# Kernel optimization log

Hardware: AMD Instinct MI355X
Metric: run time of the kernel (lower is better)

The kernel has to match this reference:

```python
import jax, jax.numpy as jnp
import numpy as np

NUM_EXPERTS = 64
N_GROUP = 8
TOPK_GROUP = 4
TOPK = 8
EPG = NUM_EXPERTS // N_GROUP  # experts per group


def setup_inputs() -> dict:
    key = jax.random.key(0)
    k1, k2 = jax.random.split(key)
    S, D = 16384, 2048
    x = jax.random.normal(k1, (S, D), dtype=jnp.float32)
    # nn.Linear(n_embd, num_experts, bias=False) weight: [E, D]
    W = jax.random.normal(k2, (NUM_EXPERTS, D), dtype=jnp.float32) * (1.0 / np.sqrt(D))
    e_score_correction_bias = jnp.zeros((NUM_EXPERTS,), dtype=jnp.float32)
    return {"x": x, "W": W, "e_score_correction_bias": e_score_correction_bias}


def reference(x, W, e_score_correction_bias):
    S = x.shape[0]
    E, G, K = NUM_EXPERTS, N_GROUP, TOPK
    # router projection in fp32
    logits = jnp.einsum('sd,ed->se', x.astype(jnp.float32), W)  # [S, E]
    scores = jax.nn.sigmoid(logits).astype(x.dtype)             # [S, E]
    scores_biased = scores + e_score_correction_bias            # [S, E]
    # group max over experts-per-group
    group_scores = scores_biased.reshape(S, G, EPG).max(axis=-1)  # [S, G]
    _, selected_group = jax.lax.top_k(group_scores, TOPK_GROUP)   # [S, topk_group]
    # build group mask via scatter (faithful to scatter_ of ones)
    group_mask = jnp.zeros((S, G), dtype=scores_biased.dtype)
    group_mask = group_mask.at[jnp.arange(S)[:, None], selected_group].set(1.0)
    expert_mask = jnp.broadcast_to(group_mask[:, :, None], (S, G, EPG)).reshape(S, E)
    scores_masked = jnp.where(expert_mask == 0, -jnp.inf, scores_biased)
    _, topk_idx = jax.lax.top_k(scores_masked, K)               # [S, K]
    final_weights = jnp.take_along_axis(scores, topk_idx, axis=1)  # [S, K]
    # norm_topk_prob=True
    final_weights = final_weights / (final_weights.sum(axis=-1, keepdims=True) + 1e-20)
    return (topk_idx, final_weights)
```

## Files before the change

### kernel.cpp

```cpp
#include <hip/hip_runtime.h>
#include <math.h>

#define N_EXP 64
#define TOPK 8
#define TOPK_G 4
#define D_DIM 2048
#define S_TOT 16384
#define RPB 64
#define NBUF 4
#define NCH 32

typedef _Float16 half8 __attribute__((ext_vector_type(8)));
typedef float f32x4 __attribute__((ext_vector_type(4)));

typedef __attribute__((address_space(1))) const unsigned int ga_u32;
typedef __attribute__((address_space(3))) unsigned int ls_u32;
#define GLL(src, dst) \
    __builtin_amdgcn_global_load_lds((ga_u32*)(src), (ls_u32*)(dst), 16, 0, 0)
#define VM(n) asm volatile("s_waitcnt vmcnt(" #n ")" ::: "memory")
#define BAR() do { asm volatile("" ::: "memory"); \
                   __builtin_amdgcn_s_barrier(); \
                   asm volatile("" ::: "memory"); } while (0)

__global__ void split_w_kernel(const float* __restrict__ W,
                               _Float16* __restrict__ wsg) {
    int t = blockIdx.x * blockDim.x + threadIdx.x;
    if (t >= 16384) return;
    const int c   = t >> 9;
    const int kh  = (t >> 8) & 1;
    const int t4  = (t >> 6) & 3;
    const int m16 = (t >> 2) & 15;
    const int kb  = t & 3;
    const int slot = (kb + (m16 >> 1)) & 3;
    _Float16* dh = wsg + (size_t)c * 8192 + (kh * 4 + t4) * 512 + m16 * 32 + slot * 8;
    _Float16* dl = dh + 4096;
    const float* s = W + (size_t)(t4 * 16 + m16) * D_DIM + c * 64 + kh * 32 + kb * 8;
#pragma unroll
    for (int i = 0; i < 8; ++i) {
        float f = s[i];
        _Float16 h = (_Float16)f;
        dh[i] = h;
        dl[i] = (_Float16)((f - (float)h) * 2048.0f);
    }
}

__launch_bounds__(1024)
__global__ void router_kernel(const float* __restrict__ x,
                              const _Float16* __restrict__ wsg,
                              const float* __restrict__ bias,
                              float* __restrict__ out_idx,
                              float* __restrict__ out_w)
{
    __shared__ __align__(16) float    xs[NBUF][4096];
    __shared__ __align__(16) _Float16 wh[NBUF][8192];

    const int tid  = threadIdx.x;
    const int w    = tid >> 6;
    const int et   = w & 3;
    const int kh   = (w >> 2) & 1;
    const int rh   = w >> 3;
    const int lane = tid & 63;
    const int m16  = lane & 15;
    const int kb   = lane >> 4;
    const int row0 = blockIdx.x * RPB;

    const int gidx = tid;
    const int gr = gidx >> 4;
    const int gs = gidx & 15;
    const int gh = gs >> 3;
    const int gq = ((gs & 7) - gr) & 7;
    const float*    xsrc = x + (size_t)(row0 + gr) * D_DIM + gh * 32 + gq * 4;
    const _Float16* wsrc = wsg + (size_t)tid * 8;

#define STAGE(c, b) do { \
        GLL(xsrc + (size_t)(c) * 64, &xs[b][w * 256]); \
        GLL(wsrc + (size_t)(c) * 8192, &wh[b][w * 512]); \
    } while (0)

    f32x4 accHH[2], accHL[2], accLH[2];
#pragma unroll
    for (int mt = 0; mt < 2; ++mt) {
        accHH[mt] = (f32x4)0.0f; accHL[mt] = (f32x4)0.0f; accLH[mt] = (f32x4)0.0f;
    }

#define COMPUTE(b) do { \
        const int boff = (kh * 4 + et) * 512 + m16 * 32 + ((kb + (m16 >> 1)) & 3) * 8; \
        const half8 bh = *(const half8*)&wh[b][boff]; \
        const half8 bl = *(const half8*)&wh[b][4096 + boff]; \
        _Pragma("unroll") \
        for (int mt = 0; mt < 2; ++mt) { \
            const int rr = rh * 32 + mt * 16 + m16; \
            const int p0 = rr * 16 + kh * 8 + ((kb * 2 + rr) & 7); \
            const int p1 = rr * 16 + kh * 8 + ((kb * 2 + 1 + rr) & 7); \
            const float4 f0 = *(const float4*)&xs[b][p0 * 4]; \
            const float4 f1 = *(const float4*)&xs[b][p1 * 4]; \
            const float v[8] = {f0.x, f0.y, f0.z, f0.w, f1.x, f1.y, f1.z, f1.w}; \
            half8 xh, xl; \
            _Pragma("unroll") \
            for (int i = 0; i < 8; ++i) { \
                _Float16 h = (_Float16)v[i]; \
                xh[i] = h; \
                xl[i] = (_Float16)((v[i] - (float)h) * 2048.0f); \
            } \
            accHH[mt] = __builtin_amdgcn_mfma_f32_16x16x32_f16(xh, bh, accHH[mt], 0, 0, 0); \
            accHL[mt] = __builtin_amdgcn_mfma_f32_16x16x32_f16(xh, bl, accHL[mt], 0, 0, 0); \
            accLH[mt] = __builtin_amdgcn_mfma_f32_16x16x32_f16(xl, bh, accLH[mt], 0, 0, 0); \
        } \
    } while (0)

    STAGE(0, 0); STAGE(1, 1);

    for (int c = 0; c < NCH; ++c) {
        if (c + 2 < NCH)        { STAGE(c + 2, (c + 2) & 3); VM(4); }
        else if (c == NCH - 2)  VM(2);
        else                    VM(0);
        BAR();
        COMPUTE(c & 3);
    }
#undef STAGE
#undef COMPUTE
    BAR();

    float* lgp = (float*)&xs[0][0];
    float* bsp = lgp + RPB * 68;

    if (tid < N_EXP) bsp[tid] = bias[tid];

    const float inv2048 = 1.0f / 2048.0f;
    if (kh == 0) {
#pragma unroll
        for (int mt = 0; mt < 2; ++mt)
#pragma unroll
            for (int r = 0; r < 4; ++r)
                lgp[(rh * 32 + mt * 16 + kb * 4 + r) * 68 + et * 16 + m16] =
                    accHH[mt][r] + (accHL[mt][r] + accLH[mt][r]) * inv2048;
    }
    __syncthreads();
    if (kh == 1) {
#pragma unroll
        for (int mt = 0; mt < 2; ++mt)
#pragma unroll
            for (int r = 0; r < 4; ++r)
                lgp[(rh * 32 + mt * 16 + kb * 4 + r) * 68 + et * 16 + m16] +=
                    accHH[mt][r] + (accHL[mt][r] + accLH[mt][r]) * inv2048;
    }
    __syncthreads();

    if (tid < RPB * 8) {
        const int rg = tid >> 3, sl = tid & 7;
#pragma unroll
        for (int j = 0; j < 8; ++j) {
            const int idx = rg * 68 + sl * 8 + j;
            lgp[idx] = 1.0f / (1.0f + expf(-lgp[idx]));
        }
    }
    __syncthreads();

    if (tid < RPB * 8) {
        const int rg = tid >> 3;
        const int sl = tid & 7;
        const int row = row0 + rg;

        float bsc[8];
        float gm = -INFINITY;
#pragma unroll
        for (int j = 0; j < 8; ++j) {
            bsc[j] = lgp[rg * 68 + sl * 8 + j] + bsp[sl * 8 + j];
            gm = fmaxf(gm, bsc[j]);
        }

        int grank = 0;
#pragma unroll
        for (int s = 1; s < 8; ++s) {
            float og = __shfl_xor(gm, s, 8);
            int   osl = sl ^ s;
            if (og > gm || (og == gm && osl < sl)) ++grank;
        }
        unsigned alive = (grank < TOPK_G) ? 0xFFu : 0u;

        float wsum = 0.f;
        float myw = 0.f;
        const int orow = row * TOPK;
        for (int k = 0; k < TOPK; ++k) {
            float bv = -INFINITY; int be = 9999;
#pragma unroll
            for (int j = 0; j < 8; ++j) {
                if (alive & (1u << j)) {
                    if (bsc[j] > bv) { bv = bsc[j]; be = sl * 8 + j; }
                }
            }
#pragma unroll
            for (int s = 1; s < 8; s <<= 1) {
                float ov = __shfl_xor(bv, s, 8);
                int   oe = __shfl_xor(be, s, 8);
                if (ov > bv || (ov == bv && oe < be)) { bv = ov; be = oe; }
            }
            const float wr = lgp[rg * 68 + be];
            wsum += wr;
            if ((be >> 3) == sl) alive &= ~(1u << (be & 7));
            if (sl == k) { out_idx[orow + k] = (float)be; myw = wr; }
        }
        const float inv = 1.0f / (wsum + 1e-20f);
        out_w[orow + sl] = myw * inv;
    }
}

extern "C" void kernel_launch(void* const* d_in, const int* in_sizes, int n_in,
                              void* d_out, int out_size, void* d_ws, size_t ws_size,
                              hipStream_t stream) {
    const float* x    = (const float*)d_in[0];
    const float* W    = (const float*)d_in[1];
    const float* bias = (const float*)d_in[2];
    float* out = (float*)d_out;
    _Float16* wsg = (_Float16*)d_ws;

    hipLaunchKernelGGL(split_w_kernel, dim3(16384 / 256), dim3(256),
                       0, stream, W, wsg);
    hipLaunchKernelGGL(router_kernel, dim3(S_TOT / RPB), dim3(1024),
                       0, stream, x, wsg, bias, out, out + S_TOT * TOPK);
}
```

Before: 42.17 us.

## Restructure router GEMM tiling: wider K chunks, per-wave 16 rows x all experts

Each pipeline chunk now covers 128 K columns instead of 64, halving the number of chunks and barriers, and buffering drops from four stages to two with a trailing barrier per iteration. The warp decomposition changes from (expert tile, K half, row half) to (16-row tile, K quarter), so each wave converts its x fragment to split fp16 once and reuses it across four expert tiles instead of converting twice per chunk. The final reduction grows from two K partials to four, serialized through shared memory. The cost is shallower prefetch, which exposes more load latency, an extra barrier per chunk, and more accumulator registers.

```diff
diff --git a/kernel.cpp b/kernel.cpp
--- a/kernel.cpp
+++ b/kernel.cpp
@@ -7,8 +7,8 @@
 #define D_DIM 2048
 #define S_TOT 16384
 #define RPB 64
-#define NBUF 4
-#define NCH 32
+#define NBUF 2
+#define NCH 16
 
 typedef _Float16 half8 __attribute__((ext_vector_type(8)));
 typedef float f32x4 __attribute__((ext_vector_type(4)));
@@ -26,15 +26,15 @@
                                _Float16* __restrict__ wsg) {
     int t = blockIdx.x * blockDim.x + threadIdx.x;
     if (t >= 16384) return;
-    const int c   = t >> 9;
-    const int kh  = (t >> 8) & 1;
+    const int c   = t >> 10;
+    const int q   = (t >> 8) & 3;
     const int t4  = (t >> 6) & 3;
     const int m16 = (t >> 2) & 15;
     const int kb  = t & 3;
     const int slot = (kb + (m16 >> 1)) & 3;
-    _Float16* dh = wsg + (size_t)c * 8192 + (kh * 4 + t4) * 512 + m16 * 32 + slot * 8;
-    _Float16* dl = dh + 4096;
-    const float* s = W + (size_t)(t4 * 16 + m16) * D_DIM + c * 64 + kh * 32 + kb * 8;
+    _Float16* dh = wsg + (size_t)c * 16384 + (q * 4 + t4) * 512 + m16 * 32 + slot * 8;
+    _Float16* dl = dh + 8192;
+    const float* s = W + (size_t)(t4 * 16 + m16) * D_DIM + c * 128 + q * 32 + kb * 8;
 #pragma unroll
     for (int i = 0; i < 8; ++i) {
         float f = s[i];
@@ -51,75 +51,76 @@
                               float* __restrict__ out_idx,
                               float* __restrict__ out_w)
 {
-    __shared__ __align__(16) float    xs[NBUF][4096];
-    __shared__ __align__(16) _Float16 wh[NBUF][8192];
+    __shared__ __align__(16) float    xs[NBUF][8192];
+    __shared__ __align__(16) _Float16 wh[NBUF][16384];
 
     const int tid  = threadIdx.x;
     const int w    = tid >> 6;
-    const int et   = w & 3;
-    const int kh   = (w >> 2) & 1;
-    const int rh   = w >> 3;
+    const int rt   = w >> 2;
+    const int kq   = w & 3;
     const int lane = tid & 63;
     const int m16  = lane & 15;
     const int kb   = lane >> 4;
     const int row0 = blockIdx.x * RPB;
 
-    const int gidx = tid;
-    const int gr = gidx >> 4;
-    const int gs = gidx & 15;
-    const int gh = gs >> 3;
-    const int gq = ((gs & 7) - gr) & 7;
-    const float*    xsrc = x + (size_t)(row0 + gr) * D_DIM + gh * 32 + gq * 4;
+    const int r1 = tid >> 5, s1 = tid & 31;
+    const int q1 = s1 >> 3, j1 = ((s1 & 7) - r1) & 7;
+    const int g2 = tid + 1024;
+    const int r2 = g2 >> 5, s2 = g2 & 31;
+    const int q2 = s2 >> 3, j2 = ((s2 & 7) - r2) & 7;
+    const float* xsrc1 = x + (size_t)(row0 + r1) * D_DIM + q1 * 32 + j1 * 4;
+    const float* xsrc2 = x + (size_t)(row0 + r2) * D_DIM + q2 * 32 + j2 * 4;
     const _Float16* wsrc = wsg + (size_t)tid * 8;
 
 #define STAGE(c, b) do { \
-        GLL(xsrc + (size_t)(c) * 64, &xs[b][w * 256]); \
-        GLL(wsrc + (size_t)(c) * 8192, &wh[b][w * 512]); \
+        GLL(xsrc1 + (size_t)(c) * 128, &xs[b][w * 256]); \
+        GLL(xsrc2 + (size_t)(c) * 128, &xs[b][4096 + w * 256]); \
+        GLL(wsrc + (size_t)(c) * 16384,        &wh[b][w * 512]); \
+        GLL(wsrc + (size_t)(c) * 16384 + 8192, &wh[b][8192 + w * 512]); \
     } while (0)
 
-    f32x4 accHH[2], accHL[2], accLH[2];
-#pragma unroll
-    for (int mt = 0; mt < 2; ++mt) {
-        accHH[mt] = (f32x4)0.0f; accHL[mt] = (f32x4)0.0f; accLH[mt] = (f32x4)0.0f;
+    f32x4 accHH[4], accHL[4], accLH[4];
+#pragma unroll
+    for (int et = 0; et < 4; ++et) {
+        accHH[et] = (f32x4)0.0f; accHL[et] = (f32x4)0.0f; accLH[et] = (f32x4)0.0f;
     }
 
 #define COMPUTE(b) do { \
-        const int boff = (kh * 4 + et) * 512 + m16 * 32 + ((kb + (m16 >> 1)) & 3) * 8; \
-        const half8 bh = *(const half8*)&wh[b][boff]; \
-        const half8 bl = *(const half8*)&wh[b][4096 + boff]; \
+        const int rr = rt * 16 + m16; \
+        const int p0 = rr * 32 + kq * 8 + ((kb * 2 + rr) & 7); \
+        const int p1 = rr * 32 + kq * 8 + ((kb * 2 + 1 + rr) & 7); \
+        const float4 f0 = *(const float4*)&xs[b][p0 * 4]; \
+        const float4 f1 = *(const float4*)&xs[b][p1 * 4]; \
+        const float v[8] = {f0.x, f0.y, f0.z, f0.w, f1.x, f1.y, f1.z, f1.w}; \
+        half8 xh, xl; \
         _Pragma("unroll") \
-        for (int mt = 0; mt < 2; ++mt) { \
-            const int rr = rh * 32 + mt * 16 + m16; \
-            const int p0 = rr * 16 + kh * 8 + ((kb * 2 + rr) & 7); \
-            const int p1 = rr * 16 + kh * 8 + ((kb * 2 + 1 + rr) & 7); \
-            const float4 f0 = *(const float4*)&xs[b][p0 * 4]; \
-            const float4 f1 = *(const float4*)&xs[b][p1 * 4]; \
-            const float v[8] = {f0.x, f0.y, f0.z, f0.w, f1.x, f1.y, f1.z, f1.w}; \
-            half8 xh, xl; \
-            _Pragma("unroll") \
-            for (int i = 0; i < 8; ++i) { \
-                _Float16 h = (_Float16)v[i]; \
-                xh[i] = h; \
-                xl[i] = (_Float16)((v[i] - (float)h) * 2048.0f); \
-            } \
-            accHH[mt] = __builtin_amdgcn_mfma_f32_16x16x32_f16(xh, bh, accHH[mt], 0, 0, 0); \
-            accHL[mt] = __builtin_amdgcn_mfma_f32_16x16x32_f16(xh, bl, accHL[mt], 0, 0, 0); \
-            accLH[mt] = __builtin_amdgcn_mfma_f32_16x16x32_f16(xl, bh, accLH[mt], 0, 0, 0); \
+        for (int i = 0; i < 8; ++i) { \
+            _Float16 h = (_Float16)v[i]; \
+            xh[i] = h; \
+            xl[i] = (_Float16)((v[i] - (float)h) * 2048.0f); \
+        } \
+        _Pragma("unroll") \
+        for (int et = 0; et < 4; ++et) { \
+            const int boff = (kq * 4 + et) * 512 + m16 * 32 + ((kb + (m16 >> 1)) & 3) * 8; \
+            const half8 bh = *(const half8*)&wh[b][boff]; \
+            const half8 bl = *(const half8*)&wh[b][8192 + boff]; \
+            accHH[et] = __builtin_amdgcn_mfma_f32_16x16x32_f16(xh, bh, accHH[et], 0, 0, 0); \
+            accHL[et] = __builtin_amdgcn_mfma_f32_16x16x32_f16(xh, bl, accHL[et], 0, 0, 0); \
+            accLH[et] = __builtin_amdgcn_mfma_f32_16x16x32_f16(xl, bh, accLH[et], 0, 0, 0); \
         } \
     } while (0)
 
-    STAGE(0, 0); STAGE(1, 1);
+    STAGE(0, 0);
 
     for (int c = 0; c < NCH; ++c) {
-        if (c + 2 < NCH)        { STAGE(c + 2, (c + 2) & 3); VM(4); }
-        else if (c == NCH - 2)  VM(2);
-        else                    VM(0);
+        if (c + 1 < NCH) { STAGE(c + 1, (c + 1) & 1); VM(4); }
+        else             VM(0);
         BAR();
-        COMPUTE(c & 3);
+        COMPUTE(c & 1);
+        BAR();
     }
 #undef STAGE
 #undef COMPUTE
-    BAR();
 
     float* lgp = (float*)&xs[0][0];
     float* bsp = lgp + RPB * 68;
@@ -127,24 +128,21 @@
     if (tid < N_EXP) bsp[tid] = bias[tid];
 
     const float inv2048 = 1.0f / 2048.0f;
-    if (kh == 0) {
-#pragma unroll
-        for (int mt = 0; mt < 2; ++mt)
-#pragma unroll
-            for (int r = 0; r < 4; ++r)
-                lgp[(rh * 32 + mt * 16 + kb * 4 + r) * 68 + et * 16 + m16] =
-                    accHH[mt][r] + (accHL[mt][r] + accLH[mt][r]) * inv2048;
-    }
-    __syncthreads();
-    if (kh == 1) {
-#pragma unroll
-        for (int mt = 0; mt < 2; ++mt)
-#pragma unroll
-            for (int r = 0; r < 4; ++r)
-                lgp[(rh * 32 + mt * 16 + kb * 4 + r) * 68 + et * 16 + m16] +=
-                    accHH[mt][r] + (accHL[mt][r] + accLH[mt][r]) * inv2048;
-    }
-    __syncthreads();
+#pragma unroll
+    for (int p = 0; p < 4; ++p) {
+        if (kq == p) {
+#pragma unroll
+            for (int et = 0; et < 4; ++et)
+#pragma unroll
+                for (int r = 0; r < 4; ++r) {
+                    const int idx = (rt * 16 + kb * 4 + r) * 68 + et * 16 + m16;
+                    const float val = accHH[et][r] + (accHL[et][r] + accLH[et][r]) * inv2048;
+                    if (p == 0) lgp[idx] = val;
+                    else        lgp[idx] += val;
+                }
+        }
+        __syncthreads();
+    }
 
     if (tid < RPB * 8) {
         const int rg = tid >> 3, sl = tid & 7;
```

Measured after the change: 44.26 us. 1.05x slower.
